# Optimization experiments

Measured on AMD Instinct MI355X. Metric: run time of the kernel, lower is better.

Reference implementation:

```python
import jax, jax.numpy as jnp
import numpy as np

N = 50000
E = 1600000


def _gcn_norm(edge_index, num_nodes):
    # PyG gcn_norm with add_self_loops=True, edge_weight=1:
    # append self loops, deg = in-degree over dst (col), norm = d_src^-1/2 * d_dst^-1/2
    loops = jnp.arange(num_nodes, dtype=edge_index.dtype)
    src = jnp.concatenate([edge_index[0], loops])
    dst = jnp.concatenate([edge_index[1], loops])
    deg = jax.ops.segment_sum(jnp.ones_like(dst, dtype=jnp.float32), dst,
                              num_segments=num_nodes)
    dinv = jnp.where(deg > 0, jax.lax.rsqrt(deg), 0.0)
    norm = dinv[src] * dinv[dst]  # [E+N]
    return src, dst, norm


def _gcn_layer(x, W, b, src, dst, norm, num_nodes):
    h = x @ W                                  # [N, out]
    msg = h[src] * norm[:, None]               # gather + scale, [E+N, out]
    out = jax.ops.segment_sum(msg, dst, num_segments=num_nodes)
    return out + b


def setup_inputs() -> dict:
    key = jax.random.key(0)
    ks = jax.random.split(key, 10)
    d_in, d_h, d_out = 128, 128, 64
    s = lambda d: 1.0 / np.sqrt(d)
    return {
        "x": jax.random.normal(ks[0], (N, d_in), dtype=jnp.float32),
        "edge_index": jax.random.randint(ks[1], (2, E), 0, N, dtype=jnp.int64),
        "W1": jax.random.normal(ks[2], (d_in, d_h), dtype=jnp.float32) * s(d_in),
        "b1": jnp.zeros((d_h,), dtype=jnp.float32),
        "W2": jax.random.normal(ks[3], (d_h, d_h), dtype=jnp.float32) * s(d_h),
        "b2": jnp.zeros((d_h,), dtype=jnp.float32),
        "W3": jax.random.normal(ks[4], (d_h, d_h), dtype=jnp.float32) * s(d_h),
        "b3": jnp.zeros((d_h,), dtype=jnp.float32),
        "W4": jax.random.normal(ks[5], (d_h, d_out), dtype=jnp.float32) * s(d_h),
        "b4": jnp.zeros((d_out,), dtype=jnp.float32),
    }


def reference(x, edge_index, W1, b1, W2, b2, W3, b3, W4, b4):
    src, dst, norm = _gcn_norm(edge_index, N)
    h = jax.nn.relu(_gcn_layer(x, W1, b1, src, dst, norm, N))
    h = jax.nn.relu(_gcn_layer(h, W2, b2, src, dst, norm, N))
    h = jax.nn.relu(_gcn_layer(h, W3, b3, src, dst, norm, N))
    h = _gcn_layer(h, W4, b4, src, dst, norm, N)
    return h
```

## Files before the change

### kernel.cpp

```cpp
#include <hip/hip_runtime.h>
#include <hip/hip_fp16.h>

constexpr int K_DIM = 128;

typedef short bf16x8 __attribute__((ext_vector_type(8)));
typedef float f32x4 __attribute__((ext_vector_type(4)));

#define GLOAD16(g, l) __builtin_amdgcn_global_load_lds( \
    (const __attribute__((address_space(1))) void*)(g), \
    (__attribute__((address_space(3))) void*)(l), 16, 0, 0)

__device__ __forceinline__ unsigned short f2bf(float f) {
  unsigned u = __float_as_uint(f);
  u += 0x7fff + ((u >> 16) & 1);
  return (unsigned short)(u >> 16);
}
__device__ __forceinline__ float bf2f(unsigned short s) {
  return __uint_as_float(((unsigned)s) << 16);
}

__global__ void zerob_k(int* __restrict__ bcount, int NBr) {
  int t = threadIdx.x;
  if (t < NBr) bcount[t] = 0;
}

__global__ __launch_bounds__(256) void bcount_k(const int* __restrict__ dst, int E,
    int* __restrict__ bcount, int NBr) {
  __shared__ int h[256];
  const int tid = threadIdx.x;
  h[tid] = 0;
  __syncthreads();
  for (int t = blockIdx.x * 256 + tid; t < E; t += gridDim.x * 256)
    atomicAdd(&h[dst[t] >> 8], 1);
  __syncthreads();
  if (tid < NBr && h[tid]) atomicAdd(&bcount[tid], h[tid]);
}

__global__ __launch_bounds__(256) void bscan_k(const int* __restrict__ bcount,
    int* __restrict__ bstart, int* __restrict__ bcursor, int NBr) {
  __shared__ int sh[256];
  const int t = threadIdx.x;
  sh[t] = (t < NBr) ? bcount[t] : 0;
  __syncthreads();
  for (int off = 1; off < 256; off <<= 1) {
    int w = (t >= off) ? sh[t - off] : 0;
    __syncthreads();
    sh[t] += w;
    __syncthreads();
  }
  if (t < NBr) {
    int ex = t ? sh[t - 1] : 0;
    bstart[t] = ex;
    bcursor[t] = ex;
  }
  if (t == NBr - 1) bstart[NBr] = sh[t];
}

__global__ __launch_bounds__(256) void bscatter_k(const int* __restrict__ ei, int E,
    int* __restrict__ bcursor, unsigned* __restrict__ brec, int NBr) {
  __shared__ int h[256];
  __shared__ int base[256];
  const int tid = threadIdx.x;
  h[tid] = 0;
  __syncthreads();
  const int chunk = (E + gridDim.x - 1) / gridDim.x;
  const int s = blockIdx.x * chunk;
  const int e = min(E, s + chunk);
  for (int t = s + tid; t < e; t += 256) atomicAdd(&h[ei[E + t] >> 8], 1);
  __syncthreads();
  if (tid < NBr && h[tid]) base[tid] = atomicAdd(&bcursor[tid], h[tid]);
  __syncthreads();
  for (int t = s + tid; t < e; t += 256) {
    int src = ei[t];
    int d = ei[E + t];
    int bk = d >> 8;
    int p = atomicAdd(&base[bk], 1);
    brec[p] = ((unsigned)src << 8) | (unsigned)(d & 255);
  }
}

__global__ __launch_bounds__(256) void bcsr_k(const unsigned* __restrict__ brec,
    const int* __restrict__ bstart, int n, int E,
    int* __restrict__ rowptr, int* __restrict__ colidx, float* __restrict__ dinv) {
  __shared__ int s_deg[256];
  __shared__ int s_cur[256];
  __shared__ int s_lrp[257];
  const int b = blockIdx.x, tid = threadIdx.x;
  const int node0 = b << 8;
  const int LC = min(256, n - node0);
  const int rs = bstart[b], cnt = bstart[b + 1] - rs;

  s_deg[tid] = (tid < LC) ? 1 : 0;
  __syncthreads();
  for (int i = tid; i < cnt; i += 256) atomicAdd(&s_deg[brec[rs + i] & 255], 1);
  __syncthreads();
  s_cur[tid] = s_deg[tid];
  __syncthreads();
  for (int off = 1; off < 256; off <<= 1) {
    int w = (tid >= off) ? s_cur[tid - off] : 0;
    __syncthreads();
    s_cur[tid] += w;
    __syncthreads();
  }
  s_lrp[tid + 1] = s_cur[tid];
  if (tid == 0) s_lrp[0] = 0;
  __syncthreads();

  const int gbase = rs + node0;
  if (tid < LC) {
    int p = s_lrp[tid];
    colidx[gbase + p] = node0 + tid;
    s_cur[tid] = p + 1;
    rowptr[node0 + tid] = gbase + p;
    dinv[node0 + tid] = rsqrtf((float)(s_lrp[tid + 1] - p));
  }
  __syncthreads();
  for (int i = tid; i < cnt; i += 256) {
    unsigned r = brec[rs + i];
    int p = atomicAdd(&s_cur[r & 255], 1);
    colidx[gbase + p] = (int)(r >> 8);
  }
  if (b == (int)gridDim.x - 1 && tid == 0) rowptr[n] = E + n;
}

__global__ __launch_bounds__(256) void split_k(const float* __restrict__ x,
    unsigned* __restrict__ zh, unsigned* __restrict__ zl, long total4) {
  long t = (long)blockIdx.x * 256 + threadIdx.x;
  if (t >= total4) return;
  float4 v = reinterpret_cast<const float4*>(x)[t];
  unsigned short hx = f2bf(v.x), hy = f2bf(v.y), hz = f2bf(v.z), hw = f2bf(v.w);
  unsigned short lx = f2bf(v.x - bf2f(hx)), ly = f2bf(v.y - bf2f(hy));
  unsigned short lz = f2bf(v.z - bf2f(hz)), lw = f2bf(v.w - bf2f(hw));
  reinterpret_cast<uint2*>(zh)[t] = make_uint2((unsigned)hx | ((unsigned)hy << 16),
                                               (unsigned)hz | ((unsigned)hw << 16));
  reinterpret_cast<uint2*>(zl)[t] = make_uint2((unsigned)lx | ((unsigned)ly << 16),
                                               (unsigned)lz | ((unsigned)lw << 16));
}

__global__ __launch_bounds__(256) void wprep_k(
    const float* __restrict__ W1, const float* __restrict__ W2,
    const float* __restrict__ W3, const float* __restrict__ W4,
    unsigned short* __restrict__ wth, unsigned short* __restrict__ wtl) {
  int id = blockIdx.x * 256 + threadIdx.x;
  if (id >= 57344) return;
  const float* W;
  int nout, base, rem;
  if (id < 49152) {
    int l = id / 16384;
    W = (l == 0) ? W1 : (l == 1) ? W2 : W3;
    nout = 128;
    base = l * 16384;
    rem = id - base;
  } else {
    W = W4;
    nout = 64;
    base = 49152;
    rem = id - base;
  }
  int k = rem / nout, c = rem % nout;
  float w = W[k * nout + c];
  unsigned short hi = f2bf(w);
  unsigned short lo = f2bf(w - bf2f(hi));
  wth[base + c * 128 + k] = hi;
  wtl[base + c * 128 + k] = lo;
}

template<int NOUT>
__global__ __launch_bounds__(256) void gemm_mfma_k(
    const unsigned short* __restrict__ Zh, const unsigned short* __restrict__ Zl,
    const unsigned short* __restrict__ Wh, const unsigned short* __restrict__ Wl,
    __half* __restrict__ H, int n) {
  constexpr int NT = NOUT / 16;
  __shared__ unsigned short Ah[128][32];
  __shared__ unsigned short Al[128][32];
  __shared__ unsigned short Bh[NOUT][32];
  __shared__ unsigned short Bl[NOUT][32];
  const int tid = threadIdx.x;
  const int lane = tid & 63;
  const int w = tid >> 6;
  const int r16 = lane & 15;
  const int kb = lane >> 4;
  const int row0 = blockIdx.x * 128;

  f32x4 acc[2][NT];
  #pragma unroll
  for (int rg = 0; rg < 2; ++rg)
    #pragma unroll
    for (int t = 0; t < NT; ++t)
      #pragma unroll
      for (int q = 0; q < 4; ++q) acc[rg][t][q] = 0.f;

  char* AhB = (char*)&Ah[0][0];
  char* AlB = (char*)&Al[0][0];
  char* BhB = (char*)&Bh[0][0];
  char* BlB = (char*)&Bl[0][0];

  for (int kc = 0; kc < 128; kc += 32) {
    __syncthreads();
    {
      int i0 = tid, i1 = tid + 256;
      int r0c = row0 + (i0 >> 2); r0c = (r0c < n) ? r0c : (n - 1);
      int r1c = row0 + (i1 >> 2); r1c = (r1c < n) ? r1c : (n - 1);
      const unsigned short* g0h = Zh + (size_t)r0c * 128 + kc + (i0 & 3) * 8;
      const unsigned short* g1h = Zh + (size_t)r1c * 128 + kc + (i1 & 3) * 8;
      const unsigned short* g0l = Zl + (size_t)r0c * 128 + kc + (i0 & 3) * 8;
      const unsigned short* g1l = Zl + (size_t)r1c * 128 + kc + (i1 & 3) * 8;
      GLOAD16(g0h, AhB + w * 1024);
      GLOAD16(g1h, AhB + 4096 + w * 1024);
      GLOAD16(g0l, AlB + w * 1024);
      GLOAD16(g1l, AlB + 4096 + w * 1024);
    }
    {
      int i0 = tid;
      const unsigned short* g0h = Wh + (size_t)(i0 >> 2) * 128 + kc + (i0 & 3) * 8;
      const unsigned short* g0l = Wl + (size_t)(i0 >> 2) * 128 + kc + (i0 & 3) * 8;
      GLOAD16(g0h, BhB + w * 1024);
      GLOAD16(g0l, BlB + w * 1024);
      if constexpr (NOUT == 128) {
        int i1 = tid + 256;
        const unsigned short* g1h = Wh + (size_t)(i1 >> 2) * 128 + kc + (i1 & 3) * 8;
        const unsigned short* g1l = Wl + (size_t)(i1 >> 2) * 128 + kc + (i1 & 3) * 8;
        GLOAD16(g1h, BhB + 4096 + w * 1024);
        GLOAD16(g1l, BlB + 4096 + w * 1024);
      }
    }
    __syncthreads();

    bf16x8 ah0 = *(const bf16x8*)&Ah[w * 32 + r16][kb * 8];
    bf16x8 ah1 = *(const bf16x8*)&Ah[w * 32 + 16 + r16][kb * 8];
    bf16x8 al0 = *(const bf16x8*)&Al[w * 32 + r16][kb * 8];
    bf16x8 al1 = *(const bf16x8*)&Al[w * 32 + 16 + r16][kb * 8];
    #pragma unroll
    for (int t = 0; t < NT; ++t) {
      bf16x8 bh = *(const bf16x8*)&Bh[t * 16 + r16][kb * 8];
      bf16x8 bl = *(const bf16x8*)&Bl[t * 16 + r16][kb * 8];
      acc[0][t] = __builtin_amdgcn_mfma_f32_16x16x32_bf16(ah0, bh, acc[0][t], 0, 0, 0);
      acc[0][t] = __builtin_amdgcn_mfma_f32_16x16x32_bf16(ah0, bl, acc[0][t], 0, 0, 0);
      acc[0][t] = __builtin_amdgcn_mfma_f32_16x16x32_bf16(al0, bh, acc[0][t], 0, 0, 0);
      acc[1][t] = __builtin_amdgcn_mfma_f32_16x16x32_bf16(ah1, bh, acc[1][t], 0, 0, 0);
      acc[1][t] = __builtin_amdgcn_mfma_f32_16x16x32_bf16(ah1, bl, acc[1][t], 0, 0, 0);
      acc[1][t] = __builtin_amdgcn_mfma_f32_16x16x32_bf16(al1, bh, acc[1][t], 0, 0, 0);
    }
  }

  #pragma unroll
  for (int rg = 0; rg < 2; ++rg) {
    #pragma unroll
    for (int t = 0; t < NT; ++t) {
      int col = t * 16 + r16;
      #pragma unroll
      for (int q = 0; q < 4; ++q) {
        int grow = row0 + w * 32 + rg * 16 + kb * 4 + q;
        if (grow < n) H[(size_t)grow * NOUT + col] = __float2half(acc[rg][t][q]);
      }
    }
  }
}

__global__ __launch_bounds__(256) void agg128_k(const __half* __restrict__ H,
    const int* __restrict__ rowptr, const int* __restrict__ colidx,
    const float* __restrict__ dinv, const float* __restrict__ bias,
    unsigned* __restrict__ Zh, unsigned* __restrict__ Zl, int n) {
  const int wave = threadIdx.x >> 6;
  const int lane = threadIdx.x & 63;
  const int node = blockIdx.x * 4 + wave;
  if (node >= n) return;
  const int s = rowptr[node], e = rowptr[node + 1];
  const __half2* H2 = reinterpret_cast<const __half2*>(H);

  float ax = 0.f, ay = 0.f;
  int m = e - s;
  int c = colidx[s + ((lane < m) ? lane : 0)];
  float dv = (lane < m) ? dinv[c] : 0.f;
  for (int base = s; base < e;) {
    int nb = base + 64;
    int kmax = e - base;
    if (kmax > 64) kmax = 64;
    int c_n = 0;
    float dv_n = 0.f;
    if (nb < e) {
      int m2 = e - nb;
      c_n = colidx[nb + ((lane < m2) ? lane : 0)];
      dv_n = (lane < m2) ? dinv[c_n] : 0.f;
    }
    int k = 0;
    for (; k + 7 < kmax; k += 8) {
      int cc[8];
      float dd[8];
      float2 hh[8];
      #pragma unroll
      for (int u = 0; u < 8; ++u) { cc[u] = __shfl(c, k + u); dd[u] = __shfl(dv, k + u); }
      #pragma unroll
      for (int u = 0; u < 8; ++u) hh[u] = __half22float2(H2[(size_t)cc[u] * 64 + lane]);
      #pragma unroll
      for (int u = 0; u < 8; ++u) { ax = fmaf(dd[u], hh[u].x, ax); ay = fmaf(dd[u], hh[u].y, ay); }
    }
    for (; k < kmax; ++k) {
      int ck = __shfl(c, k);
      float dk = __shfl(dv, k);
      float2 h = __half22float2(H2[(size_t)ck * 64 + lane]);
      ax = fmaf(dk, h.x, ax);
      ay = fmaf(dk, h.y, ay);
    }
    base = nb;
    c = c_n;
    dv = dv_n;
  }
  float di = dinv[node];
  float2 b2 = reinterpret_cast<const float2*>(bias)[lane];
  float ox = fmaxf(fmaf(di, ax, b2.x), 0.f);
  float oy = fmaxf(fmaf(di, ay, b2.y), 0.f);
  unsigned short hx = f2bf(ox), hy = f2bf(oy);
  unsigned short lx = f2bf(ox - bf2f(hx)), ly = f2bf(oy - bf2f(hy));
  Zh[(size_t)node * 64 + lane] = (unsigned)hx | ((unsigned)hy << 16);
  Zl[(size_t)node * 64 + lane] = (unsigned)lx | ((unsigned)ly << 16);
}

__global__ __launch_bounds__(256) void agg64_k(const __half* __restrict__ H,
    const int* __restrict__ rowptr, const int* __restrict__ colidx,
    const float* __restrict__ dinv, const float* __restrict__ bias,
    float* __restrict__ out, int n) {
  const int wave = threadIdx.x >> 6;
  const int lane = threadIdx.x & 63;
  const int node = blockIdx.x * 4 + wave;
  if (node >= n) return;
  const int s = rowptr[node], e = rowptr[node + 1];

  float a0 = 0.f;
  int m = e - s;
  int c = colidx[s + ((lane < m) ? lane : 0)];
  float dv = (lane < m) ? dinv[c] : 0.f;
  for (int base = s; base < e;) {
    int nb = base + 64;
    int kmax = e - base;
    if (kmax > 64) kmax = 64;
    int c_n = 0;
    float dv_n = 0.f;
    if (nb < e) {
      int m2 = e - nb;
      c_n = colidx[nb + ((lane < m2) ? lane : 0)];
      dv_n = (lane < m2) ? dinv[c_n] : 0.f;
    }
    int k = 0;
    for (; k + 7 < kmax; k += 8) {
      int cc[8];
      float dd[8];
      float hh[8];
      #pragma unroll
      for (int u = 0; u < 8; ++u) { cc[u] = __shfl(c, k + u); dd[u] = __shfl(dv, k + u); }
      #pragma unroll
      for (int u = 0; u < 8; ++u) hh[u] = __half2float(H[(size_t)cc[u] * 64 + lane]);
      #pragma unroll
      for (int u = 0; u < 8; ++u) a0 = fmaf(dd[u], hh[u], a0);
    }
    for (; k < kmax; ++k) {
      int ck = __shfl(c, k);
      float dk = __shfl(dv, k);
      a0 = fmaf(dk, __half2float(H[(size_t)ck * 64 + lane]), a0);
    }
    base = nb;
    c = c_n;
    dv = dv_n;
  }
  out[(size_t)node * 64 + lane] = fmaf(dinv[node], a0, bias[lane]);
}

extern "C" void kernel_launch(void* const* d_in, const int* in_sizes, int n_in,
                              void* d_out, int out_size, void* d_ws, size_t ws_size,
                              hipStream_t stream) {
  const int n = in_sizes[0] / K_DIM;
  const int E = in_sizes[1] / 2;
  const int NBr = (n + 255) >> 8;

  const float* x  = (const float*)d_in[0];
  const int*   ei = (const int*)d_in[1];
  const float* W1 = (const float*)d_in[2];
  const float* b1 = (const float*)d_in[3];
  const float* W2 = (const float*)d_in[4];
  const float* b2 = (const float*)d_in[5];
  const float* W3 = (const float*)d_in[6];
  const float* b3 = (const float*)d_in[7];
  const float* W4 = (const float*)d_in[8];
  const float* b4 = (const float*)d_in[9];
  float* out = (float*)d_out;

  char* ws = (char*)d_ws;
  size_t off = 0;
  auto alloc = [&](size_t bytes) -> void* {
    void* p = ws + off;
    off += (bytes + 255) & ~(size_t)255;
    return p;
  };
  int*      bcount  = (int*)     alloc(256 * 4);
  int*      bstart  = (int*)     alloc(257 * 4);
  int*      bcursor = (int*)     alloc(256 * 4);
  unsigned* brec    = (unsigned*)alloc((size_t)E * 4);
  int*      rowptr  = (int*)     alloc((size_t)(n + 1) * 4);
  int*      colidx  = (int*)     alloc((size_t)(E + n) * 4);
  float*    dinv    = (float*)   alloc((size_t)n * 4);
  unsigned short* Zh = (unsigned short*)alloc((size_t)n * 128 * 2);
  unsigned short* Zl = (unsigned short*)alloc((size_t)n * 128 * 2);
  __half*   hH      = (__half*)  alloc((size_t)n * 128 * 2);
  unsigned short* wth = (unsigned short*)alloc((size_t)57344 * 2);
  unsigned short* wtl = (unsigned short*)alloc((size_t)57344 * 2);

  zerob_k<<<1, 256, 0, stream>>>(bcount, NBr);
  bcount_k<<<512, 256, 0, stream>>>(ei + E, E, bcount, NBr);
  bscan_k<<<1, 256, 0, stream>>>(bcount, bstart, bcursor, NBr);
  bscatter_k<<<256, 256, 0, stream>>>(ei, E, bcursor, brec, NBr);
  bcsr_k<<<NBr, 256, 0, stream>>>(brec, bstart, n, E, rowptr, colidx, dinv);

  const long total4 = (long)n * 32;
  split_k<<<(int)((total4 + 255) / 256), 256, 0, stream>>>(x, (unsigned*)Zh, (unsigned*)Zl, total4);
  wprep_k<<<224, 256, 0, stream>>>(W1, W2, W3, W4, wth, wtl);

  const int gb = (n + 127) / 128;
  const int ab = (n + 3) / 4;

  gemm_mfma_k<128><<<gb, 256, 0, stream>>>(Zh, Zl, wth, wtl, hH, n);
  agg128_k<<<ab, 256, 0, stream>>>(hH, rowptr, colidx, dinv, b1, (unsigned*)Zh, (unsigned*)Zl, n);
  gemm_mfma_k<128><<<gb, 256, 0, stream>>>(Zh, Zl, wth + 16384, wtl + 16384, hH, n);
  agg128_k<<<ab, 256, 0, stream>>>(hH, rowptr, colidx, dinv, b2, (unsigned*)Zh, (unsigned*)Zl, n);
  gemm_mfma_k<128><<<gb, 256, 0, stream>>>(Zh, Zl, wth + 32768, wtl + 32768, hH, n);
  agg128_k<<<ab, 256, 0, stream>>>(hH, rowptr, colidx, dinv, b3, (unsigned*)Zh, (unsigned*)Zl, n);
  gemm_mfma_k<64><<<gb, 256, 0, stream>>>(Zh, Zl, wth + 49152, wtl + 49152, hH, n);
  agg64_k<<<ab, 256, 0, stream>>>(hH, rowptr, colidx, dinv, b4, out, n);
}
```

Measured before the change: 326.8 us.

## Fold source dinv scaling into GEMM epilogue and vectorize edge gather

The GEMM epilogue now multiplies each output row by dinv of its source node, so the aggregation no longer gathers dinv per neighbor. The aggregation kernel is rewritten so each wave processes four edges at once, with 16 lanes each loading a 16-byte chunk of a row, then reduces the four partial sums with cross-lane shuffles. Outputs are written with nontemporal vector stores. This cuts dependent dinv gathers and issues wider loads per edge, at the cost of a cross-lane reduction and more idle lanes on low-degree nodes.

```diff
diff --git a/kernel.cpp b/kernel.cpp
--- a/kernel.cpp
+++ b/kernel.cpp
@@ -5,6 +5,8 @@
 
 typedef short bf16x8 __attribute__((ext_vector_type(8)));
 typedef float f32x4 __attribute__((ext_vector_type(4)));
+typedef unsigned uint4e __attribute__((ext_vector_type(4)));
+typedef float float4e __attribute__((ext_vector_type(4)));
 
 #define GLOAD16(g, l) __builtin_amdgcn_global_load_lds( \
     (const __attribute__((address_space(1))) void*)(g), \
@@ -169,7 +171,7 @@
 __global__ __launch_bounds__(256) void gemm_mfma_k(
     const unsigned short* __restrict__ Zh, const unsigned short* __restrict__ Zl,
     const unsigned short* __restrict__ Wh, const unsigned short* __restrict__ Wl,
-    __half* __restrict__ H, int n) {
+    const float* __restrict__ dinv, __half* __restrict__ H, int n) {
   constexpr int NT = NOUT / 16;
   __shared__ unsigned short Ah[128][32];
   __shared__ unsigned short Al[128][32];
@@ -246,123 +248,101 @@
   #pragma unroll
   for (int rg = 0; rg < 2; ++rg) {
     #pragma unroll
-    for (int t = 0; t < NT; ++t) {
-      int col = t * 16 + r16;
-      #pragma unroll
-      for (int q = 0; q < 4; ++q) {
-        int grow = row0 + w * 32 + rg * 16 + kb * 4 + q;
-        if (grow < n) H[(size_t)grow * NOUT + col] = __float2half(acc[rg][t][q]);
+    for (int q = 0; q < 4; ++q) {
+      int grow = row0 + w * 32 + rg * 16 + kb * 4 + q;
+      if (grow < n) {
+        float dsc = dinv[grow];
+        #pragma unroll
+        for (int t = 0; t < NT; ++t)
+          H[(size_t)grow * NOUT + t * 16 + r16] = __float2half(dsc * acc[rg][t][q]);
       }
     }
   }
 }
 
-__global__ __launch_bounds__(256) void agg128_k(const __half* __restrict__ H,
+template<int NOUT, bool LAST>
+__global__ __launch_bounds__(256) void agg_k(const __half* __restrict__ H,
     const int* __restrict__ rowptr, const int* __restrict__ colidx,
     const float* __restrict__ dinv, const float* __restrict__ bias,
-    unsigned* __restrict__ Zh, unsigned* __restrict__ Zl, int n) {
-  const int wave = threadIdx.x >> 6;
-  const int lane = threadIdx.x & 63;
-  const int node = blockIdx.x * 4 + wave;
-  if (node >= n) return;
-  const int s = rowptr[node], e = rowptr[node + 1];
-  const __half2* H2 = reinterpret_cast<const __half2*>(H);
-
-  float ax = 0.f, ay = 0.f;
-  int m = e - s;
-  int c = colidx[s + ((lane < m) ? lane : 0)];
-  float dv = (lane < m) ? dinv[c] : 0.f;
-  for (int base = s; base < e;) {
-    int nb = base + 64;
-    int kmax = e - base;
-    if (kmax > 64) kmax = 64;
-    int c_n = 0;
-    float dv_n = 0.f;
-    if (nb < e) {
-      int m2 = e - nb;
-      c_n = colidx[nb + ((lane < m2) ? lane : 0)];
-      dv_n = (lane < m2) ? dinv[c_n] : 0.f;
-    }
-    int k = 0;
-    for (; k + 7 < kmax; k += 8) {
-      int cc[8];
-      float dd[8];
-      float2 hh[8];
-      #pragma unroll
-      for (int u = 0; u < 8; ++u) { cc[u] = __shfl(c, k + u); dd[u] = __shfl(dv, k + u); }
-      #pragma unroll
-      for (int u = 0; u < 8; ++u) hh[u] = __half22float2(H2[(size_t)cc[u] * 64 + lane]);
-      #pragma unroll
-      for (int u = 0; u < 8; ++u) { ax = fmaf(dd[u], hh[u].x, ax); ay = fmaf(dd[u], hh[u].y, ay); }
-    }
-    for (; k < kmax; ++k) {
-      int ck = __shfl(c, k);
-      float dk = __shfl(dv, k);
-      float2 h = __half22float2(H2[(size_t)ck * 64 + lane]);
-      ax = fmaf(dk, h.x, ax);
-      ay = fmaf(dk, h.y, ay);
-    }
-    base = nb;
-    c = c_n;
-    dv = dv_n;
-  }
-  float di = dinv[node];
-  float2 b2 = reinterpret_cast<const float2*>(bias)[lane];
-  float ox = fmaxf(fmaf(di, ax, b2.x), 0.f);
-  float oy = fmaxf(fmaf(di, ay, b2.y), 0.f);
-  unsigned short hx = f2bf(ox), hy = f2bf(oy);
-  unsigned short lx = f2bf(ox - bf2f(hx)), ly = f2bf(oy - bf2f(hy));
-  Zh[(size_t)node * 64 + lane] = (unsigned)hx | ((unsigned)hy << 16);
-  Zl[(size_t)node * 64 + lane] = (unsigned)lx | ((unsigned)ly << 16);
-}
-
-__global__ __launch_bounds__(256) void agg64_k(const __half* __restrict__ H,
-    const int* __restrict__ rowptr, const int* __restrict__ colidx,
-    const float* __restrict__ dinv, const float* __restrict__ bias,
+    unsigned* __restrict__ Zh, unsigned* __restrict__ Zl,
     float* __restrict__ out, int n) {
   const int wave = threadIdx.x >> 6;
   const int lane = threadIdx.x & 63;
   const int node = blockIdx.x * 4 + wave;
   if (node >= n) return;
+  const int fl = lane & 15;
+  const int g = lane >> 4;
   const int s = rowptr[node], e = rowptr[node + 1];
-
-  float a0 = 0.f;
-  int m = e - s;
-  int c = colidx[s + ((lane < m) ? lane : 0)];
-  float dv = (lane < m) ? dinv[c] : 0.f;
-  for (int base = s; base < e;) {
-    int nb = base + 64;
-    int kmax = e - base;
-    if (kmax > 64) kmax = 64;
-    int c_n = 0;
-    float dv_n = 0.f;
-    if (nb < e) {
-      int m2 = e - nb;
-      c_n = colidx[nb + ((lane < m2) ? lane : 0)];
-      dv_n = (lane < m2) ? dinv[c_n] : 0.f;
-    }
-    int k = 0;
-    for (; k + 7 < kmax; k += 8) {
-      int cc[8];
-      float dd[8];
-      float hh[8];
+  constexpr int NF = NOUT / 16;
+
+  float acc[NF];
+  #pragma unroll
+  for (int u = 0; u < NF; ++u) acc[u] = 0.f;
+
+  const char* Hb = reinterpret_cast<const char*>(H);
+
+  for (int base = s; base < e; base += 32) {
+    int idx = base + (lane & 31);
+    int c32 = __builtin_nontemporal_load(&colidx[(idx < e) ? idx : (e - 1)]);
+    #pragma unroll
+    for (int j = 0; j < 8; ++j) {
+      int eid = base + 4 * j + g;
+      int ck = __shfl(c32, 4 * j + g);
+      if (eid < e) {
+        if constexpr (NOUT == 128) {
+          uint4 hv = *reinterpret_cast<const uint4*>(Hb + (size_t)ck * 256 + fl * 16);
+          float2 f0 = __half22float2(*(const __half2*)&hv.x);
+          float2 f1 = __half22float2(*(const __half2*)&hv.y);
+          float2 f2 = __half22float2(*(const __half2*)&hv.z);
+          float2 f3 = __half22float2(*(const __half2*)&hv.w);
+          acc[0] += f0.x; acc[1] += f0.y; acc[2] += f1.x; acc[3] += f1.y;
+          acc[4] += f2.x; acc[5] += f2.y; acc[6] += f3.x; acc[7] += f3.y;
+        } else {
+          uint2 hv = *reinterpret_cast<const uint2*>(Hb + (size_t)ck * 128 + fl * 8);
+          float2 f0 = __half22float2(*(const __half2*)&hv.x);
+          float2 f1 = __half22float2(*(const __half2*)&hv.y);
+          acc[0] += f0.x; acc[1] += f0.y; acc[2] += f1.x; acc[3] += f1.y;
+        }
+      }
+    }
+  }
+
+  #pragma unroll
+  for (int u = 0; u < NF; ++u) {
+    acc[u] += __shfl_xor(acc[u], 16);
+    acc[u] += __shfl_xor(acc[u], 32);
+  }
+
+  if (g == 0) {
+    float d = dinv[node];
+    if constexpr (!LAST) {
+      float o[8];
       #pragma unroll
-      for (int u = 0; u < 8; ++u) { cc[u] = __shfl(c, k + u); dd[u] = __shfl(dv, k + u); }
+      for (int u = 0; u < 8; ++u)
+        o[u] = fmaxf(fmaf(d, acc[u], bias[fl * 8 + u]), 0.f);
+      uint4e vh, vl;
       #pragma unroll
-      for (int u = 0; u < 8; ++u) hh[u] = __half2float(H[(size_t)cc[u] * 64 + lane]);
-      #pragma unroll
-      for (int u = 0; u < 8; ++u) a0 = fmaf(dd[u], hh[u], a0);
-    }
-    for (; k < kmax; ++k) {
-      int ck = __shfl(c, k);
-      float dk = __shfl(dv, k);
-      a0 = fmaf(dk, __half2float(H[(size_t)ck * 64 + lane]), a0);
-    }
-    base = nb;
-    c = c_n;
-    dv = dv_n;
-  }
-  out[(size_t)node * 64 + lane] = fmaf(dinv[node], a0, bias[lane]);
+      for (int u = 0; u < 4; ++u) {
+        unsigned short h0 = f2bf(o[2 * u]), h1 = f2bf(o[2 * u + 1]);
+        unsigned short l0 = f2bf(o[2 * u] - bf2f(h0));
+        unsigned short l1 = f2bf(o[2 * u + 1] - bf2f(h1));
+        vh[u] = (unsigned)h0 | ((unsigned)h1 << 16);
+        vl[u] = (unsigned)l0 | ((unsigned)l1 << 16);
+      }
+      __builtin_nontemporal_store(vh,
+          reinterpret_cast<uint4e*>(Zh + (size_t)node * 64) + fl);
+      __builtin_nontemporal_store(vl,
+          reinterpret_cast<uint4e*>(Zl + (size_t)node * 64) + fl);
+    } else {
+      float4e o4;
+      o4[0] = fmaf(d, acc[0], bias[fl * 4 + 0]);
+      o4[1] = fmaf(d, acc[1], bias[fl * 4 + 1]);
+      o4[2] = fmaf(d, acc[2], bias[fl * 4 + 2]);
+      o4[3] = fmaf(d, acc[3], bias[fl * 4 + 3]);
+      __builtin_nontemporal_store(o4,
+          reinterpret_cast<float4e*>(out) + (size_t)node * 16 + fl);
+    }
+  }
 }
 
 extern "C" void kernel_launch(void* const* d_in, const int* in_sizes, int n_in,
@@ -417,12 +397,12 @@
   const int gb = (n + 127) / 128;
   const int ab = (n + 3) / 4;
 
-  gemm_mfma_k<128><<<gb, 256, 0, stream>>>(Zh, Zl, wth, wtl, hH, n);
-  agg128_k<<<ab, 256, 0, stream>>>(hH, rowptr, colidx, dinv, b1, (unsigned*)Zh, (unsigned*)Zl, n);
-  gemm_mfma_k<128><<<gb, 256, 0, stream>>>(Zh, Zl, wth + 16384, wtl + 16384, hH, n);
-  agg128_k<<<ab, 256, 0, stream>>>(hH, rowptr, colidx, dinv, b2, (unsigned*)Zh, (unsigned*)Zl, n);
-  gemm_mfma_k<128><<<gb, 256, 0, stream>>>(Zh, Zl, wth + 32768, wtl + 32768, hH, n);
-  agg128_k<<<ab, 256, 0, stream>>>(hH, rowptr, colidx, dinv, b3, (unsigned*)Zh, (unsigned*)Zl, n);
-  gemm_mfma_k<64><<<gb, 256, 0, stream>>>(Zh, Zl, wth + 49152, wtl + 49152, hH, n);
-  agg64_k<<<ab, 256, 0, stream>>>(hH, rowptr, colidx, dinv, b4, out, n);
-}
+  gemm_mfma_k<128><<<gb, 256, 0, stream>>>(Zh, Zl, wth, wtl, dinv, hH, n);
+  agg_k<128, false><<<ab, 256, 0, stream>>>(hH, rowptr, colidx, dinv, b1, (unsigned*)Zh, (unsigned*)Zl, nullptr, n);
+  gemm_mfma_k<128><<<gb, 256, 0, stream>>>(Zh, Zl, wth + 16384, wtl + 16384, dinv, hH, n);
+  agg_k<128, false><<<ab, 256, 0, stream>>>(hH, rowptr, colidx, dinv, b2, (unsigned*)Zh, (unsigned*)Zl, nullptr, n);
+  gemm_mfma_k<128><<<gb, 256, 0, stream>>>(Zh, Zl, wth + 32768, wtl + 32768, dinv, hH, n);
+  agg_k<128, false><<<ab, 256, 0, stream>>>(hH, rowptr, colidx, dinv, b3, (unsigned*)Zh, (unsigned*)Zl, nullptr, n);
+  gemm_mfma_k<64><<<gb, 256, 0, stream>>>(Zh, Zl, wth + 49152, wtl + 49152, dinv, hH, n);
+  agg_k<64, true><<<ab, 256, 0, stream>>>(hH, rowptr, colidx, dinv, b4, nullptr, nullptr, out, n);
+}
```

Measured after the change: 343.3 us. +5.0%, slower.

## Fold source-degree scaling into GEMM epilogue and simplify aggregation loops

Applied to the files above, without the earlier changes.

The GEMM epilogue now multiplies each output row by dinv[row] before storing to fp16. The aggregation kernels can then plain-sum neighbor rows without gathering dinv per edge, which removes a random gather and a shuffle per neighbor. The GEMM tile shrinks from 128 to 64 rows per block, doubling the grid and cutting per-wave accumulators. The colidx prefetch of the next chunk is dropped, and nontemporal loads and stores are used for colidx and outputs.

```diff
diff --git a/kernel.cpp b/kernel.cpp
--- a/kernel.cpp
+++ b/kernel.cpp
@@ -5,6 +5,7 @@
 
 typedef short bf16x8 __attribute__((ext_vector_type(8)));
 typedef float f32x4 __attribute__((ext_vector_type(4)));
+typedef unsigned uint4e __attribute__((ext_vector_type(4)));
 
 #define GLOAD16(g, l) __builtin_amdgcn_global_load_lds( \
     (const __attribute__((address_space(1))) void*)(g), \
@@ -169,10 +170,10 @@
 __global__ __launch_bounds__(256) void gemm_mfma_k(
     const unsigned short* __restrict__ Zh, const unsigned short* __restrict__ Zl,
     const unsigned short* __restrict__ Wh, const unsigned short* __restrict__ Wl,
-    __half* __restrict__ H, int n) {
+    const float* __restrict__ dinv, __half* __restrict__ H, int n) {
   constexpr int NT = NOUT / 16;
-  __shared__ unsigned short Ah[128][32];
-  __shared__ unsigned short Al[128][32];
+  __shared__ unsigned short Ah[64][32];
+  __shared__ unsigned short Al[64][32];
   __shared__ unsigned short Bh[NOUT][32];
   __shared__ unsigned short Bl[NOUT][32];
   const int tid = threadIdx.x;
@@ -180,15 +181,13 @@
   const int w = tid >> 6;
   const int r16 = lane & 15;
   const int kb = lane >> 4;
-  const int row0 = blockIdx.x * 128;
-
-  f32x4 acc[2][NT];
+  const int row0 = blockIdx.x * 64;
+
+  f32x4 acc[NT];
   #pragma unroll
-  for (int rg = 0; rg < 2; ++rg)
+  for (int t = 0; t < NT; ++t)
     #pragma unroll
-    for (int t = 0; t < NT; ++t)
-      #pragma unroll
-      for (int q = 0; q < 4; ++q) acc[rg][t][q] = 0.f;
+    for (int q = 0; q < 4; ++q) acc[t][q] = 0.f;
 
   char* AhB = (char*)&Ah[0][0];
   char* AlB = (char*)&Al[0][0];
@@ -198,61 +197,47 @@
   for (int kc = 0; kc < 128; kc += 32) {
     __syncthreads();
     {
-      int i0 = tid, i1 = tid + 256;
-      int r0c = row0 + (i0 >> 2); r0c = (r0c < n) ? r0c : (n - 1);
-      int r1c = row0 + (i1 >> 2); r1c = (r1c < n) ? r1c : (n - 1);
-      const unsigned short* g0h = Zh + (size_t)r0c * 128 + kc + (i0 & 3) * 8;
-      const unsigned short* g1h = Zh + (size_t)r1c * 128 + kc + (i1 & 3) * 8;
-      const unsigned short* g0l = Zl + (size_t)r0c * 128 + kc + (i0 & 3) * 8;
-      const unsigned short* g1l = Zl + (size_t)r1c * 128 + kc + (i1 & 3) * 8;
-      GLOAD16(g0h, AhB + w * 1024);
-      GLOAD16(g1h, AhB + 4096 + w * 1024);
-      GLOAD16(g0l, AlB + w * 1024);
-      GLOAD16(g1l, AlB + 4096 + w * 1024);
+      int rc = row0 + (tid >> 2); rc = (rc < n) ? rc : (n - 1);
+      const unsigned short* gh = Zh + (size_t)rc * 128 + kc + (tid & 3) * 8;
+      const unsigned short* gl = Zl + (size_t)rc * 128 + kc + (tid & 3) * 8;
+      GLOAD16(gh, AhB + w * 1024);
+      GLOAD16(gl, AlB + w * 1024);
     }
     {
-      int i0 = tid;
-      const unsigned short* g0h = Wh + (size_t)(i0 >> 2) * 128 + kc + (i0 & 3) * 8;
-      const unsigned short* g0l = Wl + (size_t)(i0 >> 2) * 128 + kc + (i0 & 3) * 8;
-      GLOAD16(g0h, BhB + w * 1024);
-      GLOAD16(g0l, BlB + w * 1024);
+      const unsigned short* gh = Wh + (size_t)(tid >> 2) * 128 + kc + (tid & 3) * 8;
+      const unsigned short* gl = Wl + (size_t)(tid >> 2) * 128 + kc + (tid & 3) * 8;
+      GLOAD16(gh, BhB + w * 1024);
+      GLOAD16(gl, BlB + w * 1024);
       if constexpr (NOUT == 128) {
         int i1 = tid + 256;
-        const unsigned short* g1h = Wh + (size_t)(i1 >> 2) * 128 + kc + (i1 & 3) * 8;
-        const unsigned short* g1l = Wl + (size_t)(i1 >> 2) * 128 + kc + (i1 & 3) * 8;
-        GLOAD16(g1h, BhB + 4096 + w * 1024);
-        GLOAD16(g1l, BlB + 4096 + w * 1024);
+        const unsigned short* gh1 = Wh + (size_t)(i1 >> 2) * 128 + kc + (i1 & 3) * 8;
+        const unsigned short* gl1 = Wl + (size_t)(i1 >> 2) * 128 + kc + (i1 & 3) * 8;
+        GLOAD16(gh1, BhB + 4096 + w * 1024);
+        GLOAD16(gl1, BlB + 4096 + w * 1024);
       }
     }
     __syncthreads();
 
-    bf16x8 ah0 = *(const bf16x8*)&Ah[w * 32 + r16][kb * 8];
-    bf16x8 ah1 = *(const bf16x8*)&Ah[w * 32 + 16 + r16][kb * 8];
-    bf16x8 al0 = *(const bf16x8*)&Al[w * 32 + r16][kb * 8];
-    bf16x8 al1 = *(const bf16x8*)&Al[w * 32 + 16 + r16][kb * 8];
+    bf16x8 ah = *(const bf16x8*)&Ah[w * 16 + r16][kb * 8];
+    bf16x8 al = *(const bf16x8*)&Al[w * 16 + r16][kb * 8];
     #pragma unroll
     for (int t = 0; t < NT; ++t) {
       bf16x8 bh = *(const bf16x8*)&Bh[t * 16 + r16][kb * 8];
       bf16x8 bl = *(const bf16x8*)&Bl[t * 16 + r16][kb * 8];
-      acc[0][t] = __builtin_amdgcn_mfma_f32_16x16x32_bf16(ah0, bh, acc[0][t], 0, 0, 0);
-      acc[0][t] = __builtin_amdgcn_mfma_f32_16x16x32_bf16(ah0, bl, acc[0][t], 0, 0, 0);
-      acc[0][t] = __builtin_amdgcn_mfma_f32_16x16x32_bf16(al0, bh, acc[0][t], 0, 0, 0);
-      acc[1][t] = __builtin_amdgcn_mfma_f32_16x16x32_bf16(ah1, bh, acc[1][t], 0, 0, 0);
-      acc[1][t] = __builtin_amdgcn_mfma_f32_16x16x32_bf16(ah1, bl, acc[1][t], 0, 0, 0);
-      acc[1][t] = __builtin_amdgcn_mfma_f32_16x16x32_bf16(al1, bh, acc[1][t], 0, 0, 0);
+      acc[t] = __builtin_amdgcn_mfma_f32_16x16x32_bf16(ah, bh, acc[t], 0, 0, 0);
+      acc[t] = __builtin_amdgcn_mfma_f32_16x16x32_bf16(ah, bl, acc[t], 0, 0, 0);
+      acc[t] = __builtin_amdgcn_mfma_f32_16x16x32_bf16(al, bh, acc[t], 0, 0, 0);
     }
   }
 
   #pragma unroll
-  for (int rg = 0; rg < 2; ++rg) {
-    #pragma unroll
-    for (int t = 0; t < NT; ++t) {
-      int col = t * 16 + r16;
-      #pragma unroll
-      for (int q = 0; q < 4; ++q) {
-        int grow = row0 + w * 32 + rg * 16 + kb * 4 + q;
-        if (grow < n) H[(size_t)grow * NOUT + col] = __float2half(acc[rg][t][q]);
-      }
+  for (int q = 0; q < 4; ++q) {
+    int grow = row0 + w * 16 + kb * 4 + q;
+    if (grow < n) {
+      float dsc = dinv[grow];
+      #pragma unroll
+      for (int t = 0; t < NT; ++t)
+        H[(size_t)grow * NOUT + t * 16 + r16] = __float2half(dsc * acc[t][q]);
     }
   }
 }
@@ -269,51 +254,38 @@
   const __half2* H2 = reinterpret_cast<const __half2*>(H);
 
   float ax = 0.f, ay = 0.f;
-  int m = e - s;
-  int c = colidx[s + ((lane < m) ? lane : 0)];
-  float dv = (lane < m) ? dinv[c] : 0.f;
-  for (int base = s; base < e;) {
-    int nb = base + 64;
-    int kmax = e - base;
-    if (kmax > 64) kmax = 64;
-    int c_n = 0;
-    float dv_n = 0.f;
-    if (nb < e) {
-      int m2 = e - nb;
-      c_n = colidx[nb + ((lane < m2) ? lane : 0)];
-      dv_n = (lane < m2) ? dinv[c_n] : 0.f;
-    }
+  for (int base = s; base < e; base += 64) {
+    int m = e - base;
+    int c = __builtin_nontemporal_load(&colidx[base + ((lane < m) ? lane : 0)]);
+    int kmax = (m < 64) ? m : 64;
     int k = 0;
     for (; k + 7 < kmax; k += 8) {
       int cc[8];
-      float dd[8];
       float2 hh[8];
       #pragma unroll
-      for (int u = 0; u < 8; ++u) { cc[u] = __shfl(c, k + u); dd[u] = __shfl(dv, k + u); }
+      for (int u = 0; u < 8; ++u) cc[u] = __shfl(c, k + u);
       #pragma unroll
       for (int u = 0; u < 8; ++u) hh[u] = __half22float2(H2[(size_t)cc[u] * 64 + lane]);
       #pragma unroll
-      for (int u = 0; u < 8; ++u) { ax = fmaf(dd[u], hh[u].x, ax); ay = fmaf(dd[u], hh[u].y, ay); }
+      for (int u = 0; u < 8; ++u) { ax += hh[u].x; ay += hh[u].y; }
     }
     for (; k < kmax; ++k) {
       int ck = __shfl(c, k);
-      float dk = __shfl(dv, k);
       float2 h = __half22float2(H2[(size_t)ck * 64 + lane]);
-      ax = fmaf(dk, h.x, ax);
-      ay = fmaf(dk, h.y, ay);
-    }
-    base = nb;
-    c = c_n;
-    dv = dv_n;
-  }
-  float di = dinv[node];
+      ax += h.x;
+      ay += h.y;
+    }
+  }
+  float d = dinv[node];
   float2 b2 = reinterpret_cast<const float2*>(bias)[lane];
-  float ox = fmaxf(fmaf(di, ax, b2.x), 0.f);
-  float oy = fmaxf(fmaf(di, ay, b2.y), 0.f);
+  float ox = fmaxf(fmaf(d, ax, b2.x), 0.f);
+  float oy = fmaxf(fmaf(d, ay, b2.y), 0.f);
   unsigned short hx = f2bf(ox), hy = f2bf(oy);
   unsigned short lx = f2bf(ox - bf2f(hx)), ly = f2bf(oy - bf2f(hy));
-  Zh[(size_t)node * 64 + lane] = (unsigned)hx | ((unsigned)hy << 16);
-  Zl[(size_t)node * 64 + lane] = (unsigned)lx | ((unsigned)ly << 16);
+  unsigned vh = (unsigned)hx | ((unsigned)hy << 16);
+  unsigned vl = (unsigned)lx | ((unsigned)ly << 16);
+  __builtin_nontemporal_store(vh, &Zh[(size_t)node * 64 + lane]);
+  __builtin_nontemporal_store(vl, &Zl[(size_t)node * 64 + lane]);
 }
 
 __global__ __launch_bounds__(256) void agg64_k(const __half* __restrict__ H,
@@ -327,42 +299,28 @@
   const int s = rowptr[node], e = rowptr[node + 1];
 
   float a0 = 0.f;
-  int m = e - s;
-  int c = colidx[s + ((lane < m) ? lane : 0)];
-  float dv = (lane < m) ? dinv[c] : 0.f;
-  for (int base = s; base < e;) {
-    int nb = base + 64;
-    int kmax = e - base;
-    if (kmax > 64) kmax = 64;
-    int c_n = 0;
-    float dv_n = 0.f;
-    if (nb < e) {
-      int m2 = e - nb;
-      c_n = colidx[nb + ((lane < m2) ? lane : 0)];
-      dv_n = (lane < m2) ? dinv[c_n] : 0.f;
-    }
+  for (int base = s; base < e; base += 64) {
+    int m = e - base;
+    int c = __builtin_nontemporal_load(&colidx[base + ((lane < m) ? lane : 0)]);
+    int kmax = (m < 64) ? m : 64;
     int k = 0;
     for (; k + 7 < kmax; k += 8) {
       int cc[8];
-      float dd[8];
       float hh[8];
       #pragma unroll
-      for (int u = 0; u < 8; ++u) { cc[u] = __shfl(c, k + u); dd[u] = __shfl(dv, k + u); }
+      for (int u = 0; u < 8; ++u) cc[u] = __shfl(c, k + u);
       #pragma unroll
       for (int u = 0; u < 8; ++u) hh[u] = __half2float(H[(size_t)cc[u] * 64 + lane]);
       #pragma unroll
-      for (int u = 0; u < 8; ++u) a0 = fmaf(dd[u], hh[u], a0);
+      for (int u = 0; u < 8; ++u) a0 += hh[u];
     }
     for (; k < kmax; ++k) {
       int ck = __shfl(c, k);
-      float dk = __shfl(dv, k);
-      a0 = fmaf(dk, __half2float(H[(size_t)ck * 64 + lane]), a0);
-    }
-    base = nb;
-    c = c_n;
-    dv = dv_n;
-  }
-  out[(size_t)node * 64 + lane] = fmaf(dinv[node], a0, bias[lane]);
+      a0 += __half2float(H[(size_t)ck * 64 + lane]);
+    }
+  }
+  float o = fmaf(dinv[node], a0, bias[lane]);
+  __builtin_nontemporal_store(o, &out[(size_t)node * 64 + lane]);
 }
 
 extern "C" void kernel_launch(void* const* d_in, const int* in_sizes, int n_in,
@@ -414,15 +372,15 @@
   split_k<<<(int)((total4 + 255) / 256), 256, 0, stream>>>(x, (unsigned*)Zh, (unsigned*)Zl, total4);
   wprep_k<<<224, 256, 0, stream>>>(W1, W2, W3, W4, wth, wtl);
 
-  const int gb = (n + 127) / 128;
+  const int gb = (n + 63) / 64;
   const int ab = (n + 3) / 4;
 
-  gemm_mfma_k<128><<<gb, 256, 0, stream>>>(Zh, Zl, wth, wtl, hH, n);
+  gemm_mfma_k<128><<<gb, 256, 0, stream>>>(Zh, Zl, wth, wtl, dinv, hH, n);
   agg128_k<<<ab, 256, 0, stream>>>(hH, rowptr, colidx, dinv, b1, (unsigned*)Zh, (unsigned*)Zl, n);
-  gemm_mfma_k<128><<<gb, 256, 0, stream>>>(Zh, Zl, wth + 16384, wtl + 16384, hH, n);
+  gemm_mfma_k<128><<<gb, 256, 0, stream>>>(Zh, Zl, wth + 16384, wtl + 16384, dinv, hH, n);
   agg128_k<<<ab, 256, 0, stream>>>(hH, rowptr, colidx, dinv, b2, (unsigned*)Zh, (unsigned*)Zl, n);
-  gemm_mfma_k<128><<<gb, 256, 0, stream>>>(Zh, Zl, wth + 32768, wtl + 32768, hH, n);
+  gemm_mfma_k<128><<<gb, 256, 0, stream>>>(Zh, Zl, wth + 32768, wtl + 32768, dinv, hH, n);
   agg128_k<<<ab, 256, 0, stream>>>(hH, rowptr, colidx, dinv, b3, (unsigned*)Zh, (unsigned*)Zl, n);
-  gemm_mfma_k<64><<<gb, 256, 0, stream>>>(Zh, Zl, wth + 49152, wtl + 49152, hH, n);
+  gemm_mfma_k<64><<<gb, 256, 0, stream>>>(Zh, Zl, wth + 49152, wtl + 49152, dinv, hH, n);
   agg64_k<<<ab, 256, 0, stream>>>(hH, rowptr, colidx, dinv, b4, out, n);
 }
```

Result: no change. 324.0 us (-0.9%).
